# Kernel optimization log

Hardware: AMD Instinct MI355X
Metric: run time of the kernel (lower is better)

The kernel has to match this reference:

```python
import math
import jax, jax.numpy as jnp
import numpy as np

S = 64.0
M = 0.5
C = 1.5
K = 16
EPS = 1e-6
IN = 128
OUT = 10000
B = 1024


def _l2norm(x, axis):
    # matches torch.nn.functional.normalize (eps=1e-12)
    n = jnp.linalg.norm(x, axis=axis, keepdims=True)
    return x / jnp.maximum(n, 1e-12)


def setup_inputs() -> dict:
    key = jax.random.key(0)
    k1, k2, k3, k4 = jax.random.split(key, 4)
    inp = jax.random.normal(k1, (B, IN), dtype=jnp.float32)
    factor = jax.random.uniform(k2, (B, 1), dtype=jnp.float32)
    label = jax.random.randint(k3, (B,), 0, OUT)
    # xavier_uniform over (k, in, out): fan_in=IN, fan_out=OUT (last two dims)
    limit = math.sqrt(6.0 / (IN + OUT))
    weight = jax.random.uniform(k4, (K, IN, OUT), dtype=jnp.float32, minval=-limit, maxval=limit)
    return {"input": inp, "factor": factor, "label": label, "weight": weight}


def reference(input, factor, label, weight):
    # disguise-adaptive margin: (B,1)
    func_a = jnp.power(C, factor / 12.0) * M
    threshold = math.pi - func_a  # (B,1)

    xn = _l2norm(input, axis=1)          # (B, IN)
    wn = _l2norm(weight, axis=1)         # (K, IN, OUT), normalized along IN

    # batched sub-center matmul then max over sub-centers k
    cos_all = jnp.einsum('bf,kfo->kbo', xn, wn)   # (K, B, OUT)
    cos_theta = jnp.max(cos_all, axis=0)          # (B, OUT)

    theta = jnp.arccos(jnp.clip(cos_theta, -1.0 + EPS, 1.0 - EPS))
    one_hot = jax.nn.one_hot(label, OUT, dtype=theta.dtype)  # (B, OUT)
    selected = jnp.where(theta > threshold, jnp.zeros_like(one_hot), one_hot)
    logits = jnp.cos(jnp.where(selected.astype(bool), theta + func_a, theta)) * S

    # cross-entropy (mean reduction)
    logp = jax.nn.log_softmax(logits, axis=-1)
    cls_loss = -jnp.mean(jnp.take_along_axis(logp, label[:, None], axis=1))

    # top-1 accuracy (percent), detached stat
    pred = jnp.argmax(logits, axis=1)
    prec1 = jnp.mean((pred == label).astype(jnp.float32)) * 100.0
    return cls_loss, prec1
```

## Files before the change

kernel.cpp:

```cpp
#include <hip/hip_runtime.h>
#include <hip/hip_bf16.h>
#include <math.h>

#define BB    1024
#define FIN   128
#define NOUT  10000
#define NBLK  79
#define NCB   158
#define NK    16
#define NPART (NCB * 2)
#define LDX   136

typedef __attribute__((ext_vector_type(8))) short short8;
typedef __attribute__((ext_vector_type(4))) float floatx4;

__device__ __forceinline__ unsigned packbf(float a, float b) {
    __hip_bfloat162 h = __float22bfloat162_rn(make_float2(a, b));
    union { __hip_bfloat162 h2; unsigned u; } v;
    v.h2 = h;
    return v.u;
}

__global__ void rowprep(const float* __restrict__ X, const float* __restrict__ factor,
                        float* __restrict__ xinv, float* __restrict__ fa_out,
                        float* __restrict__ thr_out) {
    int b = blockIdx.x;
    int lane = threadIdx.x;
    float v0 = X[b * FIN + lane];
    float v1 = X[b * FIN + 64 + lane];
    float s = v0 * v0 + v1 * v1;
    #pragma unroll
    for (int off = 32; off > 0; off >>= 1) s += __shfl_down(s, off);
    if (lane == 0) {
        float n = sqrtf(s);
        xinv[b] = 1.0f / fmaxf(n, 1e-12f);
        float fa = powf(1.5f, factor[b] * (1.0f / 12.0f)) * 0.5f;
        fa_out[b] = fa;
        thr_out[b] = (float)M_PI - fa;
    }
}

__global__ __launch_bounds__(256) void wconv(
    const float* __restrict__ W, unsigned char* __restrict__ Wbf,
    const float* __restrict__ X, const float* __restrict__ factor,
    float* __restrict__ xinv, float* __restrict__ fa_out, float* __restrict__ thr_out) {

    __shared__ float xs2[128 * 64];
    __shared__ uint4 wout[1024];
    __shared__ float sq2[256];
    __shared__ float wis[64];

    const int tid = threadIdx.x;

    if (blockIdx.x >= NK * NCB) {
        int rb = blockIdx.x - NK * NCB;
        int w4 = tid >> 6, lane = tid & 63;
        for (int i = w4; i < 64; i += 4) {
            int row = rb * 64 + i;
            float v0 = X[row * FIN + lane];
            float v1 = X[row * FIN + 64 + lane];
            float s = v0 * v0 + v1 * v1;
            #pragma unroll
            for (int off = 32; off > 0; off >>= 1) s += __shfl_down(s, off);
            if (lane == 0) {
                xinv[row] = 1.0f / fmaxf(sqrtf(s), 1e-12f);
                float fa = powf(1.5f, factor[row] * (1.0f / 12.0f)) * 0.5f;
                fa_out[row] = fa;
                thr_out[row] = (float)M_PI - fa;
            }
        }
        return;
    }

    const int k  = blockIdx.x / NCB;
    const int cb = blockIdx.x - k * NCB;
    const int o0 = cb * 64;

    #pragma unroll
    for (int it = 0; it < 8; it++) {
        int idx = it * 256 + tid;
        int f  = idx >> 4;
        int c4 = idx & 15;
        int o  = o0 + c4 * 4;
        float4 v = make_float4(0.f, 0.f, 0.f, 0.f);
        if (o < NOUT)
            v = *(const float4*)(W + ((size_t)k * FIN + f) * NOUT + o);
        *(float4*)(xs2 + f * 64 + c4 * 4) = v;
    }
    __syncthreads();

    {
        const int col = tid & 63;
        const int seg = tid >> 6;
        float s = 0.0f;
        #pragma unroll 8
        for (int f2 = 0; f2 < 32; f2++) {
            float x = xs2[(seg * 32 + f2) * 64 + col];
            s = fmaf(x, x, s);
        }
        sq2[tid] = s;
    }
    __syncthreads();
    if (tid < 64)
        wis[tid] = 1.0f / fmaxf(sqrtf(sq2[tid] + sq2[tid + 64] + sq2[tid + 128] + sq2[tid + 192]), 1e-12f);
    __syncthreads();

    {
        const int c   = tid >> 2;
        const int sub = tid & 3;
        const float wi = wis[c];
        const int wn  = c >> 5;
        const int n2  = (c >> 4) & 1;
        const int l15 = c & 15;
        #pragma unroll
        for (int i = 0; i < 4; i++) {
            int tc = sub * 4 + i;
            int kk = tc >> 2;
            int q  = tc & 3;
            float v0 = xs2[(tc * 8 + 0) * 64 + c] * wi;
            float v1 = xs2[(tc * 8 + 1) * 64 + c] * wi;
            float v2 = xs2[(tc * 8 + 2) * 64 + c] * wi;
            float v3 = xs2[(tc * 8 + 3) * 64 + c] * wi;
            float v4 = xs2[(tc * 8 + 4) * 64 + c] * wi;
            float v5 = xs2[(tc * 8 + 5) * 64 + c] * wi;
            float v6 = xs2[(tc * 8 + 6) * 64 + c] * wi;
            float v7 = xs2[(tc * 8 + 7) * 64 + c] * wi;
            uint4 u;
            u.x = packbf(v0, v1);
            u.y = packbf(v2, v3);
            u.z = packbf(v4, v5);
            u.w = packbf(v6, v7);
            wout[wn * 512 + n2 * 256 + kk * 64 + q * 16 + l15] = u;
        }
    }
    __syncthreads();

    unsigned char* dst = Wbf + ((size_t)k * NCB + cb) * 16384;
    #pragma unroll
    for (int i = 0; i < 4; i++) {
        int idx = i * 256 + tid;
        *(uint4*)(dst + (size_t)idx * 16) = wout[idx];
    }
}

__global__ __launch_bounds__(256, 2) void gemm_mx(
    const float* __restrict__ X, const unsigned char* __restrict__ Wbf,
    const int* __restrict__ label, const float* __restrict__ xinv,
    float2* __restrict__ partial, float* __restrict__ cosl) {

    __shared__ short xs[64 * LDX];

    const int tid  = threadIdx.x;
    const int lane = tid & 63;
    const int w    = tid >> 6;
    const int l15  = lane & 15;
    const int q    = lane >> 4;
    const int wm   = w & 1;
    const int wn   = w >> 1;

    const int id    = blockIdx.x;
    const int group = id >> 7;
    const int sub   = id & 127;
    const int cb    = group * 8 + (sub & 7);
    const int y     = sub >> 3;
    if (cb >= NCB) return;
    const int r0 = y * 64;
    const int o0 = cb * 64;

    #pragma unroll
    for (int it = 0; it < 8; it++) {
        int idx = it * 256 + tid;
        int row = idx >> 5;
        int c4  = idx & 31;
        const float4 v = *(const float4*)(X + (size_t)(r0 + row) * FIN + c4 * 4);
        float xi = xinv[r0 + row];
        uint2 p;
        p.x = packbf(v.x * xi, v.y * xi);
        p.y = packbf(v.z * xi, v.w * xi);
        *(uint2*)(xs + row * LDX + c4 * 4) = p;
    }
    __syncthreads();

    short8 af[2][4];
    #pragma unroll
    for (int mt = 0; mt < 2; mt++)
        #pragma unroll
        for (int kk = 0; kk < 4; kk++)
            af[mt][kk] = *(const short8*)(xs + (wm * 32 + mt * 16 + l15) * LDX + kk * 32 + q * 8);

    const unsigned char* wbase = Wbf + (size_t)cb * 16384 + (size_t)wn * 8192 + (size_t)lane * 16;
    const size_t kstr = (size_t)NCB * 16384;

    auto loadk = [&](int k, short8* dst) {
        const unsigned char* p = wbase + (size_t)k * kstr;
        #pragma unroll
        for (int n2 = 0; n2 < 2; n2++)
            #pragma unroll
            for (int kk = 0; kk < 4; kk++)
                dst[n2 * 4 + kk] = *(const short8*)(p + n2 * 4096 + kk * 1024);
    };

    floatx4 maxv[2][2];
    #pragma unroll
    for (int mt = 0; mt < 2; mt++)
        #pragma unroll
        for (int n2 = 0; n2 < 2; n2++)
            #pragma unroll
            for (int r = 0; r < 4; r++)
                maxv[mt][n2][r] = -INFINITY;

    auto compute = [&](const short8* b) {
        floatx4 acc[2][2];
        #pragma unroll
        for (int mt = 0; mt < 2; mt++)
            #pragma unroll
            for (int n2 = 0; n2 < 2; n2++)
                acc[mt][n2] = (floatx4){0.f, 0.f, 0.f, 0.f};
        #pragma unroll
        for (int kk = 0; kk < 4; kk++)
            #pragma unroll
            for (int mt = 0; mt < 2; mt++)
                #pragma unroll
                for (int n2 = 0; n2 < 2; n2++)
                    acc[mt][n2] = __builtin_amdgcn_mfma_f32_16x16x32_bf16(
                        af[mt][kk], b[n2 * 4 + kk], acc[mt][n2], 0, 0, 0);
        #pragma unroll
        for (int mt = 0; mt < 2; mt++)
            #pragma unroll
            for (int n2 = 0; n2 < 2; n2++)
                #pragma unroll
                for (int r = 0; r < 4; r++)
                    maxv[mt][n2][r] = fmaxf(maxv[mt][n2][r], acc[mt][n2][r]);
    };

    short8 bA[8], bB[8];
    loadk(0, bA);
    for (int k = 0; k < NK; k += 2) {
        loadk(k + 1, bB);
        compute(bA);
        if (k + 2 < NK) loadk(k + 2, bA);
        compute(bB);
    }

    #pragma unroll
    for (int mt = 0; mt < 2; mt++) {
        #pragma unroll
        for (int rr = 0; rr < 4; rr++) {
            int row = r0 + wm * 32 + mt * 16 + q * 4 + rr;
            int lb = label[row];
            float m = -1e30f, s = 0.f;
            #pragma unroll
            for (int n2 = 0; n2 < 2; n2++) {
                int o = o0 + wn * 32 + n2 * 16 + l15;
                if (o < NOUT) {
                    float c = maxv[mt][n2][rr];
                    if (o == lb) {
                        cosl[row] = c;
                    } else {
                        float l = 64.0f * fminf(fmaxf(c, -1.0f + 1e-6f), 1.0f - 1e-6f);
                        if (l > m) { s = s * __expf(m - l) + 1.0f; m = l; }
                        else       { s += __expf(l - m); }
                    }
                }
            }
            #pragma unroll
            for (int off = 1; off <= 8; off <<= 1) {
                float m2 = __shfl_xor(m, off);
                float s2 = __shfl_xor(s, off);
                float M = fmaxf(m, m2);
                s = s * __expf(m - M) + s2 * __expf(m2 - M);
                m = M;
            }
            if (l15 == 0)
                partial[(size_t)row * NPART + cb * 2 + wn] = make_float2(m, s);
        }
    }
}

__global__ __launch_bounds__(256, 2) void gemm_stats(
    const float* __restrict__ X, const float* __restrict__ W,
    const int* __restrict__ label, const float* __restrict__ xinv,
    float2* __restrict__ partial, float* __restrict__ cosl) {

    __shared__ short xs[128 * LDX];
    __shared__ short wt[128 * LDX];
    __shared__ float sqs[128][2];

    const int tid  = threadIdx.x;
    const int lane = tid & 63;
    const int w    = tid >> 6;
    const int l15  = lane & 15;
    const int q    = lane >> 4;
    const int wm   = w & 1;
    const int wn   = w >> 1;

    const int id    = blockIdx.x;
    const int group = id >> 6;
    const int sub   = id & 63;
    const int jb    = group * 8 + (sub & 7);
    const int y     = sub >> 3;
    if (jb >= NBLK) return;
    const int r0 = y * 128;
    const int o0 = jb * 128;

    #pragma unroll
    for (int it = 0; it < 16; it++) {
        int idx = it * 256 + tid;
        int row = idx >> 5;
        int c4  = idx & 31;
        const float4 v = *(const float4*)(X + (size_t)(r0 + row) * FIN + c4 * 4);
        uint2 p;
        p.x = packbf(v.x, v.y);
        p.y = packbf(v.z, v.w);
        *(uint2*)(xs + row * LDX + c4 * 4) = p;
    }

    const int st_o = (w & 1) * 64 + lane;
    const int st_f = (w >> 1) * 64;
    const int st_h = w >> 1;
    const int go   = o0 + st_o;
    const bool ov  = go < NOUT;

    float rw[64];
    {
        const float* Wp = W + (size_t)st_f * NOUT + go;
        #pragma unroll
        for (int g = 0; g < 16; g++)
            #pragma unroll
            for (int c = 0; c < 4; c++)
                rw[g * 4 + c] = ov ? Wp[(size_t)(g * 4 + c) * NOUT] : 0.0f;
    }
    __syncthreads();

    short8 af[4][4];
    #pragma unroll
    for (int mt = 0; mt < 4; mt++)
        #pragma unroll
        for (int kk = 0; kk < 4; kk++)
            af[mt][kk] = *(const short8*)(xs + (wm * 64 + mt * 16 + l15) * LDX + kk * 32 + q * 8);

    floatx4 maxv[4][4];
    #pragma unroll
    for (int mt = 0; mt < 4; mt++)
        #pragma unroll
        for (int nt = 0; nt < 4; nt++)
            #pragma unroll
            for (int r = 0; r < 4; r++)
                maxv[mt][nt][r] = -INFINITY;

    for (int k = 0; k < NK; k++) {
        float sq = 0.0f;
        uint2 pk[16];
        #pragma unroll
        for (int g = 0; g < 16; g++) {
            float a0 = rw[g * 4 + 0], a1 = rw[g * 4 + 1];
            float a2 = rw[g * 4 + 2], a3 = rw[g * 4 + 3];
            sq = fmaf(a0, a0, sq); sq = fmaf(a1, a1, sq);
            sq = fmaf(a2, a2, sq); sq = fmaf(a3, a3, sq);
            pk[g].x = packbf(a0, a1);
            pk[g].y = packbf(a2, a3);
        }
        __syncthreads();
        #pragma unroll
        for (int g = 0; g < 16; g++)
            *(uint2*)(wt + st_o * LDX + st_f + g * 4) = pk[g];
        sqs[st_o][st_h] = sq;
        __syncthreads();

        if (k < NK - 1) {
            const float* Wn = W + ((size_t)(k + 1) * FIN + st_f) * NOUT + go;
            #pragma unroll
            for (int g = 0; g < 16; g++)
                #pragma unroll
                for (int c = 0; c < 4; c++)
                    rw[g * 4 + c] = ov ? Wn[(size_t)(g * 4 + c) * NOUT] : 0.0f;
        }

        float wv[4];
        #pragma unroll
        for (int nt = 0; nt < 4; nt++) {
            int col = wn * 64 + nt * 16 + l15;
            wv[nt] = 1.0f / fmaxf(sqrtf(sqs[col][0] + sqs[col][1]), 1e-12f);
        }

        #pragma unroll
        for (int h = 0; h < 2; h++) {
            floatx4 acc[4][2];
            #pragma unroll
            for (int mt = 0; mt < 4; mt++) {
                acc[mt][0] = (floatx4){0.f, 0.f, 0.f, 0.f};
                acc[mt][1] = (floatx4){0.f, 0.f, 0.f, 0.f};
            }
            #pragma unroll
            for (int kk = 0; kk < 4; kk++) {
                short8 bf0 = *(const short8*)(wt + (wn * 64 + (h * 2 + 0) * 16 + l15) * LDX + kk * 32 + q * 8);
                short8 bf1 = *(const short8*)(wt + (wn * 64 + (h * 2 + 1) * 16 + l15) * LDX + kk * 32 + q * 8);
                #pragma unroll
                for (int mt = 0; mt < 4; mt++) {
                    acc[mt][0] = __builtin_amdgcn_mfma_f32_16x16x32_bf16(af[mt][kk], bf0, acc[mt][0], 0, 0, 0);
                    acc[mt][1] = __builtin_amdgcn_mfma_f32_16x16x32_bf16(af[mt][kk], bf1, acc[mt][1], 0, 0, 0);
                }
            }
            #pragma unroll
            for (int mt = 0; mt < 4; mt++)
                #pragma unroll
                for (int n2 = 0; n2 < 2; n2++)
                    #pragma unroll
                    for (int r = 0; r < 4; r++)
                        maxv[mt][h * 2 + n2][r] =
                            fmaxf(maxv[mt][h * 2 + n2][r], acc[mt][n2][r] * wv[h * 2 + n2]);
        }
    }

    #pragma unroll
    for (int mt = 0; mt < 4; mt++) {
        #pragma unroll
        for (int rr = 0; rr < 4; rr++) {
            int row = r0 + wm * 64 + mt * 16 + q * 4 + rr;
            float xi = xinv[row];
            int lb = label[row];
            float m = -1e30f, s = 0.f;
            #pragma unroll
            for (int nt = 0; nt < 4; nt++) {
                int o = o0 + wn * 64 + nt * 16 + l15;
                if (o < NOUT) {
                    float c = maxv[mt][nt][rr] * xi;
                    if (o == lb) {
                        cosl[row] = c;
                    } else {
                        float l = 64.0f * fminf(fmaxf(c, -1.0f + 1e-6f), 1.0f - 1e-6f);
                        if (l > m) { s = s * __expf(m - l) + 1.0f; m = l; }
                        else       { s += __expf(l - m); }
                    }
                }
            }
            #pragma unroll
            for (int off = 1; off <= 8; off <<= 1) {
                float m2 = __shfl_xor(m, off);
                float s2 = __shfl_xor(s, off);
                float M = fmaxf(m, m2);
                s = s * __expf(m - M) + s2 * __expf(m2 - M);
                m = M;
            }
            if (l15 == 0) {
                partial[(size_t)row * NPART + jb * 4 + wn * 2 + 0] = make_float2(m, s);
                partial[(size_t)row * NPART + jb * 4 + wn * 2 + 1] = make_float2(-1e30f, 0.f);
            }
        }
    }
}

__global__ void finalize_rows(const float2* __restrict__ partial, const float* __restrict__ cosl,
                              const float* __restrict__ fa, const float* __restrict__ thr,
                              float2* __restrict__ rowres) {
    int w = threadIdx.x >> 6;
    int lane = threadIdx.x & 63;
    int b = blockIdx.x * 4 + w;
    float m = -1e30f, s = 0.0f;
    for (int j = lane; j < NPART; j += 64) {
        float2 p = partial[(size_t)b * NPART + j];
        float M = fmaxf(m, p.x);
        s = s * __expf(m - M) + p.y * __expf(p.x - M);
        m = M;
    }
    #pragma unroll
    for (int off = 1; off < 64; off <<= 1) {
        float m2 = __shfl_xor(m, off);
        float s2 = __shfl_xor(s, off);
        float M = fmaxf(m, m2);
        s = s * __expf(m - M) + s2 * __expf(m2 - M);
        m = M;
    }
    if (lane == 0) {
        float c = fminf(fmaxf(cosl[b], -1.0f + 1e-6f), 1.0f - 1e-6f);
        float theta = acosf(c);
        float ll = (theta > thr[b]) ? 64.0f * c : 64.0f * cosf(theta + fa[b]);
        float M = fmaxf(m, ll);
        float S = s * __expf(m - M) + __expf(ll - M);
        rowres[b] = make_float2(M + logf(S) - ll, (ll > m) ? 100.0f : 0.0f);
    }
}

__global__ void finalize_sum(const float2* __restrict__ rowres, float* __restrict__ out) {
    __shared__ float sl[1024];
    __shared__ float sc[1024];
    int b = threadIdx.x;
    float2 v = rowres[b];
    sl[b] = v.x;
    sc[b] = v.y;
    __syncthreads();
    for (int st = 512; st > 0; st >>= 1) {
        if (b < st) { sl[b] += sl[b + st]; sc[b] += sc[b + st]; }
        __syncthreads();
    }
    if (b == 0) {
        out[0] = sl[0] * (1.0f / 1024.0f);
        out[1] = sc[0] * (1.0f / 1024.0f);
    }
}

extern "C" void kernel_launch(void* const* d_in, const int* in_sizes, int n_in,
                              void* d_out, int out_size, void* d_ws, size_t ws_size,
                              hipStream_t stream) {
    const float* X      = (const float*)d_in[0];
    const float* factor = (const float*)d_in[1];
    const int*   label  = (const int*)d_in[2];
    const float* W      = (const float*)d_in[3];
    float* out = (float*)d_out;
    float* ws  = (float*)d_ws;

    float*  xinv = ws;
    float*  fa   = ws + 1024;
    float*  thr  = ws + 2048;
    float*  cosl = ws + 3072;
    float2* rowres = (float2*)(ws + 4096);
    float2* partial = (float2*)(ws + 6144);
    unsigned char* Wbf = (unsigned char*)d_ws + 4 * 1024 * 1024;

    const size_t wbf_bytes = (size_t)NK * NCB * 16384;
    const size_t need = 4ull * 1024 * 1024 + wbf_bytes;

    if (ws_size >= need) {
        wconv<<<NK * NCB + 16, 256, 0, stream>>>(W, Wbf, X, factor, xinv, fa, thr);
        gemm_mx<<<2560, 256, 0, stream>>>(X, Wbf, label, xinv, partial, cosl);
    } else {
        rowprep<<<BB, 64, 0, stream>>>(X, factor, xinv, fa, thr);
        gemm_stats<<<640, 256, 0, stream>>>(X, W, label, xinv, partial, cosl);
    }
    finalize_rows<<<BB / 4, 256, 0, stream>>>(partial, cosl, fa, thr, rowres);
    finalize_sum<<<1, BB, 0, stream>>>(rowres, out);
}
```

Measured before the change: 218.1 us.

## Double the row tile and stage sub-center weights through LDS via async loads

The GEMM block now covers 128 rows with 512 threads instead of 64 rows with 256, so each weight tile fetched from global memory is shared by twice as many rows. Weight tiles per sub-center are no longer loaded straight into registers. They are streamed into a double-buffered LDS area with global_load_lds async copies, and the LDS is shared with the X staging buffer through a union. The goal is to halve global weight traffic and cut register pressure. The cost is a block-wide barrier every sub-center iteration, plus extra LDS reads for the B fragments.

New measurement: 215.4 us. No clear change (-1.2%).

```diff
diff --git a/kernel.cpp b/kernel.cpp
--- a/kernel.cpp
+++ b/kernel.cpp
@@ -19,6 +19,12 @@
     union { __hip_bfloat162 h2; unsigned u; } v;
     v.h2 = h;
     return v.u;
+}
+
+__device__ __forceinline__ void async16(const void* g, void* l) {
+    __builtin_amdgcn_global_load_lds(
+        (const __attribute__((address_space(1))) unsigned int*)g,
+        (__attribute__((address_space(3))) unsigned int*)l, 16, 0, 0);
 }
 
 __global__ void rowprep(const float* __restrict__ X, const float* __restrict__ factor,
@@ -143,33 +149,36 @@
     }
 }
 
-__global__ __launch_bounds__(256, 2) void gemm_mx(
+__global__ __launch_bounds__(512, 2) void gemm_mx(
     const float* __restrict__ X, const unsigned char* __restrict__ Wbf,
     const int* __restrict__ label, const float* __restrict__ xinv,
     float2* __restrict__ partial, float* __restrict__ cosl) {
 
-    __shared__ short xs[64 * LDX];
+    __shared__ union {
+        short xs[128 * LDX];
+        short bb[2][8192];
+    } u;
 
     const int tid  = threadIdx.x;
     const int lane = tid & 63;
     const int w    = tid >> 6;
     const int l15  = lane & 15;
     const int q    = lane >> 4;
-    const int wm   = w & 1;
-    const int wn   = w >> 1;
+    const int wm   = w & 3;
+    const int wn   = w >> 2;
 
     const int id    = blockIdx.x;
-    const int group = id >> 7;
-    const int sub   = id & 127;
+    const int group = id >> 6;
+    const int sub   = id & 63;
     const int cb    = group * 8 + (sub & 7);
     const int y     = sub >> 3;
     if (cb >= NCB) return;
-    const int r0 = y * 64;
+    const int r0 = y * 128;
     const int o0 = cb * 64;
 
     #pragma unroll
     for (int it = 0; it < 8; it++) {
-        int idx = it * 256 + tid;
+        int idx = it * 512 + tid;
         int row = idx >> 5;
         int c4  = idx & 31;
         const float4 v = *(const float4*)(X + (size_t)(r0 + row) * FIN + c4 * 4);
@@ -177,7 +186,7 @@
         uint2 p;
         p.x = packbf(v.x * xi, v.y * xi);
         p.y = packbf(v.z * xi, v.w * xi);
-        *(uint2*)(xs + row * LDX + c4 * 4) = p;
+        *(uint2*)(u.xs + row * LDX + c4 * 4) = p;
     }
     __syncthreads();
 
@@ -186,19 +195,18 @@
     for (int mt = 0; mt < 2; mt++)
         #pragma unroll
         for (int kk = 0; kk < 4; kk++)
-            af[mt][kk] = *(const short8*)(xs + (wm * 32 + mt * 16 + l15) * LDX + kk * 32 + q * 8);
-
-    const unsigned char* wbase = Wbf + (size_t)cb * 16384 + (size_t)wn * 8192 + (size_t)lane * 16;
-    const size_t kstr = (size_t)NCB * 16384;
-
-    auto loadk = [&](int k, short8* dst) {
-        const unsigned char* p = wbase + (size_t)k * kstr;
-        #pragma unroll
-        for (int n2 = 0; n2 < 2; n2++)
-            #pragma unroll
-            for (int kk = 0; kk < 4; kk++)
-                dst[n2 * 4 + kk] = *(const short8*)(p + n2 * 4096 + kk * 1024);
+            af[mt][kk] = *(const short8*)(u.xs + (wm * 32 + mt * 16 + l15) * LDX + kk * 32 + q * 8);
+    __syncthreads();
+
+    auto issue = [&](int k) {
+        const unsigned char* g = Wbf + ((size_t)k * NCB + cb) * 16384
+                                 + (size_t)w * 2048 + (size_t)lane * 16;
+        short* d = u.bb[k & 1] + w * 1024;
+        async16(g, d);
+        async16(g + 1024, d + 512);
     };
+
+    issue(0);
 
     floatx4 maxv[2][2];
     #pragma unroll
@@ -209,7 +217,11 @@
             for (int r = 0; r < 4; r++)
                 maxv[mt][n2][r] = -INFINITY;
 
-    auto compute = [&](const short8* b) {
+    for (int k = 0; k < NK; k++) {
+        __syncthreads();
+        if (k < NK - 1) issue(k + 1);
+        const short* wt = u.bb[k & 1];
+
         floatx4 acc[2][2];
         #pragma unroll
         for (int mt = 0; mt < 2; mt++)
@@ -217,13 +229,18 @@
             for (int n2 = 0; n2 < 2; n2++)
                 acc[mt][n2] = (floatx4){0.f, 0.f, 0.f, 0.f};
         #pragma unroll
-        for (int kk = 0; kk < 4; kk++)
+        for (int kk = 0; kk < 4; kk++) {
+            short8 bf[2];
+            #pragma unroll
+            for (int n2 = 0; n2 < 2; n2++)
+                bf[n2] = *(const short8*)(wt + wn * 4096 + n2 * 2048 + kk * 512 + lane * 8);
             #pragma unroll
             for (int mt = 0; mt < 2; mt++)
                 #pragma unroll
                 for (int n2 = 0; n2 < 2; n2++)
                     acc[mt][n2] = __builtin_amdgcn_mfma_f32_16x16x32_bf16(
-                        af[mt][kk], b[n2 * 4 + kk], acc[mt][n2], 0, 0, 0);
+                        af[mt][kk], bf[n2], acc[mt][n2], 0, 0, 0);
+        }
         #pragma unroll
         for (int mt = 0; mt < 2; mt++)
             #pragma unroll
@@ -231,15 +248,6 @@
                 #pragma unroll
                 for (int r = 0; r < 4; r++)
                     maxv[mt][n2][r] = fmaxf(maxv[mt][n2][r], acc[mt][n2][r]);
-    };
-
-    short8 bA[8], bB[8];
-    loadk(0, bA);
-    for (int k = 0; k < NK; k += 2) {
-        loadk(k + 1, bB);
-        compute(bA);
-        if (k + 2 < NK) loadk(k + 2, bA);
-        compute(bB);
     }
 
     #pragma unroll
@@ -522,7 +530,7 @@
 
     if (ws_size >= need) {
         wconv<<<NK * NCB + 16, 256, 0, stream>>>(W, Wbf, X, factor, xinv, fa, thr);
-        gemm_mx<<<2560, 256, 0, stream>>>(X, Wbf, label, xinv, partial, cosl);
+        gemm_mx<<<1280, 512, 0, stream>>>(X, Wbf, label, xinv, partial, cosl);
     } else {
         rowprep<<<BB, 64, 0, stream>>>(X, factor, xinv, fa, thr);
         gemm_stats<<<640, 256, 0, stream>>>(X, W, label, xinv, partial, cosl);
```
